# Performance work log

Hardware: AMD Instinct MI355X
Metric: run time of the kernel (lower is better)

Reference implementation:

```python
import jax, jax.numpy as jnp
import numpy as np

B, T, D = 4, 4096, 1024


def setup_inputs() -> dict:
    key = jax.random.key(0)
    x = jax.random.normal(key, (B, T, D), dtype=jnp.float32)
    alpha = jnp.full((1,), 0.9, dtype=jnp.float32)  # fixed scalar damping (buffer)
    return {"x": x, "alpha": alpha}


def reference(x, alpha):
    # h[t] = alpha*x[t] + (1-alpha)*h[t-1], computed as causal FFT convolution
    # with exponential kernel w[tau] = alpha * (1-alpha)**tau, zero-padded to 2T.
    a = alpha.reshape(())
    Tlen = x.shape[1]
    n_fft = 2 * Tlen
    powers = jnp.arange(Tlen, dtype=x.dtype)
    kernel = a * (1.0 - a) ** powers                      # (T,)
    x_f = jnp.fft.rfft(x, n=n_fft, axis=1)                # (B, T+1, D) complex
    k_f = jnp.fft.rfft(kernel, n=n_fft)                   # (T+1,) complex
    h = jnp.fft.irfft(x_f * k_f[None, :, None], n=n_fft, axis=1)
    return h[:, :Tlen, :].astype(x.dtype)
```

## Files before the change

### kernel.cpp

```cpp
#include <hip/hip_runtime.h>


#define B_ 4
#define T_ 4096
#define D_ 1024
#define CHUNK 16
#define DB 256
#define WFIX 16

typedef float v4f __attribute__((ext_vector_type(4)));

__global__ __launch_bounds__(64)
void ema_scan_kernel(const float* __restrict__ x,
                     const float* __restrict__ alpha,
                     float* __restrict__ out) {
    const int lane    = threadIdx.x;
    const int dSplits = D_ / DB;
    const int chunk   = blockIdx.x / dSplits;
    const int dseg    = blockIdx.x % dSplits;
    const int b       = blockIdx.y;
    const int d0      = dseg * DB + lane * 4;
    const int t0      = chunk * CHUNK;

    const float a = alpha[0];
    const float r = 1.0f - a;

    int W;
    if (!(r > 0.0f)) {
        W = 0;
    } else if (r >= 1.0f) {
        W = t0;
    } else {
        W = (int)ceilf(28.0f / (-logf(r)));
        if (W < WFIX) W = WFIX;
        if (W > t0)   W = t0;
    }

    const float* xp = x   + ((size_t)b * T_ + (size_t)(t0 - W)) * D_ + d0;
    float*       op = out + ((size_t)b * T_ + (size_t)t0) * D_ + d0;

    v4f h = (v4f)(0.0f);
    v4f xv[CHUNK > WFIX ? CHUNK : WFIX];

    if (W == WFIX) {
#pragma unroll
        for (int i = 0; i < WFIX; ++i) xv[i] = *(const v4f*)(xp + (size_t)i * D_);
        xp += (size_t)WFIX * D_;
#pragma unroll
        for (int i = 0; i < WFIX; ++i) h = r * h + a * xv[i];
    } else {
        for (int i = 0; i < W; ++i) {
            v4f t = *(const v4f*)xp;
            xp += D_;
            h = r * h + a * t;
        }
    }

#pragma unroll
    for (int j = 0; j < CHUNK; ++j) xv[j] = *(const v4f*)(xp + (size_t)j * D_);
#pragma unroll
    for (int j = 0; j < CHUNK; ++j) {
        h = r * h + a * xv[j];
        __builtin_nontemporal_store(h, (v4f*)(op + (size_t)j * D_));
    }
}

extern "C" void kernel_launch(void* const* d_in, const int* in_sizes, int n_in,
                              void* d_out, int out_size, void* d_ws, size_t ws_size,
                              hipStream_t stream) {
    const float* x     = (const float*)d_in[0];
    const float* alpha = (const float*)d_in[1];
    float*       out   = (float*)d_out;

    dim3 grid((T_ / CHUNK) * (D_ / DB), B_);
    ema_scan_kernel<<<grid, 64, 0, stream>>>(x, alpha, out);
}
```

Baseline: 115.9 us.

## Double chunk length, shrink warm-up window, and double-buffer chunk loads

Each block now produces 32 time steps instead of 16 and uses a shorter warm-up window (tolerance constant lowered, minimum 8). This cuts the redundant overlap reads per output row and the total memory traffic. Chunk loads are split into groups of 8 that are double-buffered in registers, overlapping loads with the recurrence. The looser truncation tolerance slightly raises approximation error, and halving the grid lowers parallelism.

```diff
diff --git a/kernel.cpp b/kernel.cpp
--- a/kernel.cpp
+++ b/kernel.cpp
@@ -4,9 +4,11 @@
 #define B_ 4
 #define T_ 4096
 #define D_ 1024
-#define CHUNK 16
+#define CHUNK 32
 #define DB 256
-#define WFIX 16
+#define WFIX 8
+#define GRP 8
+#define NGRP (CHUNK / GRP)
 
 typedef float v4f __attribute__((ext_vector_type(4)));
 
@@ -31,7 +33,7 @@
     } else if (r >= 1.0f) {
         W = t0;
     } else {
-        W = (int)ceilf(28.0f / (-logf(r)));
+        W = (int)ceilf(18.0f / (-logf(r)));
         if (W < WFIX) W = WFIX;
         if (W > t0)   W = t0;
     }
@@ -40,28 +42,46 @@
     float*       op = out + ((size_t)b * T_ + (size_t)t0) * D_ + d0;
 
     v4f h = (v4f)(0.0f);
-    v4f xv[CHUNK > WFIX ? CHUNK : WFIX];
 
     if (W == WFIX) {
+        v4f w[WFIX];
+        v4f g[2][GRP];
+        const float* xm = xp + (size_t)WFIX * D_;
 #pragma unroll
-        for (int i = 0; i < WFIX; ++i) xv[i] = *(const v4f*)(xp + (size_t)i * D_);
-        xp += (size_t)WFIX * D_;
+        for (int i = 0; i < WFIX; ++i) w[i] = *(const v4f*)(xp + (size_t)i * D_);
 #pragma unroll
-        for (int i = 0; i < WFIX; ++i) h = r * h + a * xv[i];
+        for (int j = 0; j < GRP; ++j)  g[0][j] = *(const v4f*)(xm + (size_t)j * D_);
+
+#pragma unroll
+        for (int i = 0; i < WFIX; ++i) h = r * h + a * w[i];
+
+#pragma unroll
+        for (int gi = 0; gi < NGRP; ++gi) {
+            if (gi + 1 < NGRP) {
+                const float* xn = xm + (size_t)(gi + 1) * GRP * D_;
+#pragma unroll
+                for (int j = 0; j < GRP; ++j)
+                    g[(gi + 1) & 1][j] = *(const v4f*)(xn + (size_t)j * D_);
+            }
+#pragma unroll
+            for (int j = 0; j < GRP; ++j) {
+                h = r * h + a * g[gi & 1][j];
+                __builtin_nontemporal_store(
+                    h, (v4f*)(op + ((size_t)gi * GRP + j) * D_));
+            }
+        }
     } else {
         for (int i = 0; i < W; ++i) {
             v4f t = *(const v4f*)xp;
             xp += D_;
             h = r * h + a * t;
         }
-    }
-
-#pragma unroll
-    for (int j = 0; j < CHUNK; ++j) xv[j] = *(const v4f*)(xp + (size_t)j * D_);
-#pragma unroll
-    for (int j = 0; j < CHUNK; ++j) {
-        h = r * h + a * xv[j];
-        __builtin_nontemporal_store(h, (v4f*)(op + (size_t)j * D_));
+        for (int j = 0; j < CHUNK; ++j) {
+            v4f t = *(const v4f*)xp;
+            xp += D_;
+            h = r * h + a * t;
+            __builtin_nontemporal_store(h, (v4f*)(op + (size_t)j * D_));
+        }
     }
 }
 
```

Result: faster. 112.6 us (-2.9%).
